# Kernel optimization log

Hardware: AMD Instinct MI355X
Metric: run time of the kernel (lower is better)

Reference implementation:

```python
import jax, jax.numpy as jnp
import numpy as np

EPS = 1e-20

def setup_inputs() -> dict:
    key = jax.random.key(0)
    k1, k2 = jax.random.split(key)
    x = jax.random.normal(k1, (8192, 4096), dtype=jnp.float32)
    weight = jax.random.normal(k2, (4096, 4096), dtype=jnp.float32)  # [out, in]
    return {"x": x, "weight": weight}

def reference(x, weight):
    # Binarize activations and weights with sign(v + eps), then matmul.
    xb = jnp.sign(x + EPS)
    wb = jnp.sign(weight + EPS)
    return jnp.matmul(xb, wb.T)  # [N, out]
```

## Files before the change

kernel.cpp:

```cpp
#include <hip/hip_runtime.h>
#include <stdint.h>

#define EPSF 1e-20f

typedef __attribute__((ext_vector_type(4))) int i32x4;
typedef __attribute__((ext_vector_type(16))) int i32x16;


__global__ __launch_bounds__(256)
void bin_i8_kernel(const float4* __restrict__ src, uint32_t* __restrict__ dst,
                   int n4) {
    int base = blockIdx.x * 1024 + threadIdx.x;
#pragma unroll
    for (int j = 0; j < 4; ++j) {
        int idx = base + j * 256;
        if (idx < n4) {
            float4 v = src[idx];
            uint32_t b0 = (v.x < -EPSF) ? 0xFFu : 0x01u;
            uint32_t b1 = (v.y < -EPSF) ? 0xFFu : 0x01u;
            uint32_t b2 = (v.z < -EPSF) ? 0xFFu : 0x01u;
            uint32_t b3 = (v.w < -EPSF) ? 0xFFu : 0x01u;
            dst[idx] = b0 | (b1 << 8) | (b2 << 16) | (b3 << 24);
        }
    }
}

#define GM 128
#define GN 128
#define GK 128

__global__ __launch_bounds__(256, 3)
void i8mfma_gemm(const char* __restrict__ xi8, const char* __restrict__ wi8,
                 float* __restrict__ out) {
    __shared__ char xs[GM * GK];
    __shared__ char wsh[GN * GK];

    const int t = threadIdx.x;
    const int lane = t & 63;
    const int wave = t >> 6;
    const int wm = (wave >> 1) * 64;
    const int wn = (wave & 1) * 64;
    const int row0 = blockIdx.y * GM;
    const int col0 = blockIdx.x * GN;
    const int lrow = lane & 31;
    const int half = lane >> 5;

    i32x16 acc[2][2];
#pragma unroll
    for (int r = 0; r < 2; ++r)
#pragma unroll
        for (int c = 0; c < 2; ++c)
#pragma unroll
            for (int e = 0; e < 16; ++e) acc[r][c][e] = 0;

    for (int kc = 0; kc < 4096; kc += GK) {
        __syncthreads();
#pragma unroll
        for (int j = 0; j < 4; ++j) {
            int c = j * 256 + t;
            int row = c >> 3;
            int q = c & 7;
            int qg = q ^ (row & 7);
            const char* srcx = xi8 + (size_t)(row0 + row) * 4096 + kc + qg * 16;
            __builtin_amdgcn_global_load_lds((const uint32_t*)srcx,
                                             (uint32_t*)(xs + c * 16), 16, 0, 0);
            const char* srcw = wi8 + (size_t)(col0 + row) * 4096 + kc + qg * 16;
            __builtin_amdgcn_global_load_lds((const uint32_t*)srcw,
                                             (uint32_t*)(wsh + c * 16), 16, 0, 0);
        }
        __syncthreads();

#pragma unroll
        for (int s = 0; s < 4; ++s) {
            int g = 2 * s + half;
            i32x4 a[2], b[2];
#pragma unroll
            for (int r = 0; r < 2; ++r) {
                int row = wm + r * 32 + lrow;
                int qs = g ^ (row & 7);
                a[r] = *(const i32x4*)(xs + row * GK + qs * 16);
            }
#pragma unroll
            for (int c = 0; c < 2; ++c) {
                int col = wn + c * 32 + lrow;
                int qs = g ^ (col & 7);
                b[c] = *(const i32x4*)(wsh + col * GK + qs * 16);
            }
#pragma unroll
            for (int r = 0; r < 2; ++r)
#pragma unroll
                for (int c = 0; c < 2; ++c)
                    acc[r][c] = __builtin_amdgcn_mfma_i32_32x32x32_i8(
                        a[r], b[c], acc[r][c], 0, 0, 0);
        }
    }

#pragma unroll
    for (int r = 0; r < 2; ++r)
#pragma unroll
        for (int c = 0; c < 2; ++c)
#pragma unroll
            for (int e = 0; e < 16; ++e) {
                int rr = row0 + wm + r * 32 + (e & 3) + 8 * (e >> 2) + 4 * half;
                int cc = col0 + wn + c * 32 + lrow;
                out[(size_t)rr * 4096 + cc] = (float)acc[r][c][e];
            }
}


__global__ __launch_bounds__(256)
void binarize_kernel(const float* __restrict__ src,
                     unsigned long long* __restrict__ dst, int n256) {
    int wave = blockIdx.x * 4 + (threadIdx.x >> 6);
    if (wave >= n256) return;
    int lane = threadIdx.x & 63;
    const float4* p = (const float4*)(src + (size_t)wave * 256);
    float4 v = p[lane];
    unsigned long long m0 = __ballot(v.x < -EPSF);
    unsigned long long m1 = __ballot(v.y < -EPSF);
    unsigned long long m2 = __ballot(v.z < -EPSF);
    unsigned long long m3 = __ballot(v.w < -EPSF);
    if (lane < 4) {
        unsigned long long m = (lane == 0) ? m0 : (lane == 1) ? m1
                             : (lane == 2) ? m2 : m3;
        dst[(size_t)wave * 4 + lane] = m;
    }
}

#define BM 128
#define BN 128
#define CHUNK_Q 8
#define NCHUNK 4
#define LDSS 9

__global__ __launch_bounds__(256, 2)
void bingemm_kernel(const uint4* __restrict__ xb, const uint4* __restrict__ wb,
                    float* __restrict__ out) {
    __shared__ uint4 xsl[BM * LDSS];
    __shared__ uint4 wsl[BN * LDSS];

    const int t  = threadIdx.x;
    const int tx = t & 15;
    const int ty = t >> 4;
    const int row0 = blockIdx.y * BM;
    const int col0 = blockIdx.x * BN;

    int acc[8][8];
#pragma unroll
    for (int a = 0; a < 8; ++a)
#pragma unroll
        for (int b = 0; b < 8; ++b) acc[a][b] = 0;

    const int srow = t >> 3;
    const int sq   = t & 7;

    for (int c = 0; c < NCHUNK; ++c) {
        __syncthreads();
#pragma unroll
        for (int k = 0; k < 4; ++k) {
            int r = srow + 32 * k;
            xsl[r * LDSS + sq] = xb[(size_t)(row0 + r) * 32 + c * CHUNK_Q + sq];
            wsl[r * LDSS + sq] = wb[(size_t)(col0 + r) * 32 + c * CHUNK_Q + sq];
        }
        __syncthreads();

#pragma unroll
        for (int q = 0; q < CHUNK_Q; ++q) {
            uint4 xq[8], wq[8];
#pragma unroll
            for (int ri = 0; ri < 8; ++ri)
                xq[ri] = xsl[(ty + 16 * ri) * LDSS + q];
#pragma unroll
            for (int cj = 0; cj < 8; ++cj)
                wq[cj] = wsl[(tx + 16 * cj) * LDSS + q];
#pragma unroll
            for (int ri = 0; ri < 8; ++ri)
#pragma unroll
                for (int cj = 0; cj < 8; ++cj) {
                    acc[ri][cj] += __builtin_popcount(xq[ri].x ^ wq[cj].x);
                    acc[ri][cj] += __builtin_popcount(xq[ri].y ^ wq[cj].y);
                    acc[ri][cj] += __builtin_popcount(xq[ri].z ^ wq[cj].z);
                    acc[ri][cj] += __builtin_popcount(xq[ri].w ^ wq[cj].w);
                }
        }
    }

#pragma unroll
    for (int ri = 0; ri < 8; ++ri) {
        size_t i = row0 + ty + 16 * ri;
#pragma unroll
        for (int cj = 0; cj < 8; ++cj) {
            int j = col0 + tx + 16 * cj;
            out[i * 4096 + j] = (float)(4096 - 2 * acc[ri][cj]);
        }
    }
}

extern "C" void kernel_launch(void* const* d_in, const int* in_sizes, int n_in,
                              void* d_out, int out_size, void* d_ws, size_t ws_size,
                              hipStream_t stream) {
    const float* x = (const float*)d_in[0];
    const float* w = (const float*)d_in[1];
    float* out = (float*)d_out;

    const int M = 8192, N = 4096, K = 4096;
    const size_t need_i8 = (size_t)M * K + (size_t)N * K;

    if (ws_size >= need_i8) {
        char* xi8 = (char*)d_ws;
        char* wi8 = xi8 + (size_t)M * K;

        int n4x = (M * K) / 4;
        int n4w = (N * K) / 4;
        bin_i8_kernel<<<n4x / 1024, 256, 0, stream>>>(
            (const float4*)x, (uint32_t*)xi8, n4x);
        bin_i8_kernel<<<n4w / 1024, 256, 0, stream>>>(
            (const float4*)w, (uint32_t*)wi8, n4w);

        dim3 grid(N / GN, M / GM);
        i8mfma_gemm<<<grid, 256, 0, stream>>>(xi8, wi8, out);
    } else {
        uint32_t* xbits = (uint32_t*)d_ws;
        uint32_t* wbits = xbits + (size_t)M * (K / 32);

        binarize_kernel<<<(M * K) / 1024, 256, 0, stream>>>(
            x, (unsigned long long*)xbits, (M * K) / 256);
        binarize_kernel<<<(N * K) / 1024, 256, 0, stream>>>(
            w, (unsigned long long*)wbits, (N * K) / 256);

        dim3 grid(N / BN, M / BM);
        bingemm_kernel<<<grid, 256, 0, stream>>>(
            (const uint4*)xbits, (const uint4*)wbits, out);
    }
}
```

Baseline: 399.7 us.

## Binarize to FP4 e2m1 and use scaled f8f6f4 MFMA instead of int8

Encodes the ±1 activations and weights as 4-bit e2m1 values (0x2 = +1, 0xA = −1), packing eight per 32-bit word, which halves the workspace size and traffic. The GEMM now calls the block-scaled 32x32x64 f8f6f4 MFMA in FP4 mode with unit E8M0 scales. It accumulates in fp32, which is exact for integer sums up to 4096. Each MFMA covers twice the K depth per LDS load, so it is meant to cut both memory traffic and matrix-core issue count. The cost is relying on correct FP4 operand packing, where only the low half of the 8-int operand is used.

```diff
diff --git a/kernel.cpp b/kernel.cpp
--- a/kernel.cpp
+++ b/kernel.cpp
@@ -4,36 +4,46 @@
 #define EPSF 1e-20f
 
 typedef __attribute__((ext_vector_type(4))) int i32x4;
-typedef __attribute__((ext_vector_type(16))) int i32x16;
+typedef __attribute__((ext_vector_type(8))) int i32x8;
+typedef __attribute__((ext_vector_type(16))) float f32x16;
 
 
 __global__ __launch_bounds__(256)
-void bin_i8_kernel(const float4* __restrict__ src, uint32_t* __restrict__ dst,
-                   int n4) {
+void bin_fp4_kernel(const float4* __restrict__ src, uint32_t* __restrict__ dst,
+                    int n8) {
     int base = blockIdx.x * 1024 + threadIdx.x;
 #pragma unroll
     for (int j = 0; j < 4; ++j) {
         int idx = base + j * 256;
-        if (idx < n4) {
-            float4 v = src[idx];
-            uint32_t b0 = (v.x < -EPSF) ? 0xFFu : 0x01u;
-            uint32_t b1 = (v.y < -EPSF) ? 0xFFu : 0x01u;
-            uint32_t b2 = (v.z < -EPSF) ? 0xFFu : 0x01u;
-            uint32_t b3 = (v.w < -EPSF) ? 0xFFu : 0x01u;
-            dst[idx] = b0 | (b1 << 8) | (b2 << 16) | (b3 << 24);
+        if (idx < n8) {
+            float4 v0 = src[2 * idx];
+            float4 v1 = src[2 * idx + 1];
+            uint32_t w = 0;
+            w |= ((v0.x < -EPSF) ? 0xAu : 0x2u);
+            w |= ((v0.y < -EPSF) ? 0xAu : 0x2u) << 4;
+            w |= ((v0.z < -EPSF) ? 0xAu : 0x2u) << 8;
+            w |= ((v0.w < -EPSF) ? 0xAu : 0x2u) << 12;
+            w |= ((v1.x < -EPSF) ? 0xAu : 0x2u) << 16;
+            w |= ((v1.y < -EPSF) ? 0xAu : 0x2u) << 20;
+            w |= ((v1.z < -EPSF) ? 0xAu : 0x2u) << 24;
+            w |= ((v1.w < -EPSF) ? 0xAu : 0x2u) << 28;
+            dst[idx] = w;
         }
     }
 }
 
 #define GM 128
 #define GN 128
-#define GK 128
+#define GKB 128
+#define KB4 2048
+
+#define SCALE_ONE 0x7F7F7F7Fu
 
 __global__ __launch_bounds__(256, 3)
-void i8mfma_gemm(const char* __restrict__ xi8, const char* __restrict__ wi8,
-                 float* __restrict__ out) {
-    __shared__ char xs[GM * GK];
-    __shared__ char wsh[GN * GK];
+void fp4mfma_gemm(const char* __restrict__ x4, const char* __restrict__ w4,
+                  float* __restrict__ out) {
+    __shared__ char xs[GM * GKB];
+    __shared__ char wsh[GN * GKB];
 
     const int t = threadIdx.x;
     const int lane = t & 63;
@@ -45,15 +55,21 @@
     const int lrow = lane & 31;
     const int half = lane >> 5;
 
-    i32x16 acc[2][2];
+    f32x16 acc[2][2];
 #pragma unroll
     for (int r = 0; r < 2; ++r)
 #pragma unroll
         for (int c = 0; c < 2; ++c)
 #pragma unroll
-            for (int e = 0; e < 16; ++e) acc[r][c][e] = 0;
-
-    for (int kc = 0; kc < 4096; kc += GK) {
+            for (int e = 0; e < 16; ++e) acc[r][c][e] = 0.0f;
+
+    i32x8 a[2], b[2];
+#pragma unroll
+    for (int r = 0; r < 2; ++r)
+#pragma unroll
+        for (int e = 0; e < 8; ++e) { a[r][e] = 0; b[r][e] = 0; }
+
+    for (int kb = 0; kb < 2048; kb += GKB) {
         __syncthreads();
 #pragma unroll
         for (int j = 0; j < 4; ++j) {
@@ -61,37 +77,43 @@
             int row = c >> 3;
             int q = c & 7;
             int qg = q ^ (row & 7);
-            const char* srcx = xi8 + (size_t)(row0 + row) * 4096 + kc + qg * 16;
+            const char* srcx = x4 + (size_t)(row0 + row) * KB4 + kb + qg * 16;
             __builtin_amdgcn_global_load_lds((const uint32_t*)srcx,
                                              (uint32_t*)(xs + c * 16), 16, 0, 0);
-            const char* srcw = wi8 + (size_t)(col0 + row) * 4096 + kc + qg * 16;
+            const char* srcw = w4 + (size_t)(col0 + row) * KB4 + kb + qg * 16;
             __builtin_amdgcn_global_load_lds((const uint32_t*)srcw,
                                              (uint32_t*)(wsh + c * 16), 16, 0, 0);
         }
         __syncthreads();
 
 #pragma unroll
-        for (int s = 0; s < 4; ++s) {
-            int g = 2 * s + half;
-            i32x4 a[2], b[2];
+        for (int m = 0; m < 4; ++m) {
+            int g = 2 * m + half;
 #pragma unroll
             for (int r = 0; r < 2; ++r) {
                 int row = wm + r * 32 + lrow;
                 int qs = g ^ (row & 7);
-                a[r] = *(const i32x4*)(xs + row * GK + qs * 16);
+                i32x4 av = *(const i32x4*)(xs + row * GKB + qs * 16);
+                a[r][0] = av[0]; a[r][1] = av[1];
+                a[r][2] = av[2]; a[r][3] = av[3];
             }
 #pragma unroll
             for (int c = 0; c < 2; ++c) {
                 int col = wn + c * 32 + lrow;
                 int qs = g ^ (col & 7);
-                b[c] = *(const i32x4*)(wsh + col * GK + qs * 16);
+                i32x4 bv = *(const i32x4*)(wsh + col * GKB + qs * 16);
+                b[c][0] = bv[0]; b[c][1] = bv[1];
+                b[c][2] = bv[2]; b[c][3] = bv[3];
             }
 #pragma unroll
             for (int r = 0; r < 2; ++r)
 #pragma unroll
                 for (int c = 0; c < 2; ++c)
-                    acc[r][c] = __builtin_amdgcn_mfma_i32_32x32x32_i8(
-                        a[r], b[c], acc[r][c], 0, 0, 0);
+                    acc[r][c] = __builtin_amdgcn_mfma_scale_f32_32x32x64_f8f6f4(
+                        a[r], b[c], acc[r][c],
+                        4, 4,
+                        0, SCALE_ONE,
+                        0, SCALE_ONE);
         }
     }
 
@@ -103,7 +125,7 @@
             for (int e = 0; e < 16; ++e) {
                 int rr = row0 + wm + r * 32 + (e & 3) + 8 * (e >> 2) + 4 * half;
                 int cc = col0 + wn + c * 32 + lrow;
-                out[(size_t)rr * 4096 + cc] = (float)acc[r][c][e];
+                out[(size_t)rr * 4096 + cc] = acc[r][c][e];
             }
 }
 
@@ -204,21 +226,21 @@
     float* out = (float*)d_out;
 
     const int M = 8192, N = 4096, K = 4096;
-    const size_t need_i8 = (size_t)M * K + (size_t)N * K;
-
-    if (ws_size >= need_i8) {
-        char* xi8 = (char*)d_ws;
-        char* wi8 = xi8 + (size_t)M * K;
-
-        int n4x = (M * K) / 4;
-        int n4w = (N * K) / 4;
-        bin_i8_kernel<<<n4x / 1024, 256, 0, stream>>>(
-            (const float4*)x, (uint32_t*)xi8, n4x);
-        bin_i8_kernel<<<n4w / 1024, 256, 0, stream>>>(
-            (const float4*)w, (uint32_t*)wi8, n4w);
+    const size_t need_fp4 = ((size_t)M * K + (size_t)N * K) / 2;
+
+    if (ws_size >= need_fp4) {
+        char* x4 = (char*)d_ws;
+        char* w4 = x4 + (size_t)M * K / 2;
+
+        int n8x = (M * K) / 8;
+        int n8w = (N * K) / 8;
+        bin_fp4_kernel<<<n8x / 1024, 256, 0, stream>>>(
+            (const float4*)x, (uint32_t*)x4, n8x);
+        bin_fp4_kernel<<<n8w / 1024, 256, 0, stream>>>(
+            (const float4*)w, (uint32_t*)w4, n8w);
 
         dim3 grid(N / GN, M / GM);
-        i8mfma_gemm<<<grid, 256, 0, stream>>>(xi8, wi8, out);
+        fp4mfma_gemm<<<grid, 256, 0, stream>>>(x4, w4, out);
     } else {
         uint32_t* xbits = (uint32_t*)d_ws;
         uint32_t* wbits = xbits + (size_t)M * (K / 32);
```

After: 330.1 us. -17.4%, faster.
